# Performance work log

Hardware: AMD Instinct MI355X
Metric: run time of the kernel (lower is better)

## Reference

```python
import jax, jax.numpy as jnp
import numpy as np

NUM_ROIS = 148
BSZ = 16
HID = 64
IN_CH = 128
OUT_CH = 2
N1, E1 = 131072, 2097152
N2, E2 = 2368, 37888
LRELU_SLOPE = 0.01
BN_EPS = 1e-5


def gcn_conv(x, src, dst, ew, W, b, n):
    """PyG GCNConv with edge weights and self-loops (weight 1): D^-1/2 (A+I) D^-1/2 X W + b."""
    h = x @ W  # (n, out)
    deg = jax.ops.segment_sum(ew, dst, num_segments=n) + 1.0  # self-loop weight 1
    dinv = jax.lax.rsqrt(deg)
    norm = dinv[src] * ew * dinv[dst]  # (E,)
    out = jax.ops.segment_sum(h[src] * norm[:, None], dst, num_segments=n)
    out = out + h * (dinv * dinv)[:, None]  # self-loop term: 1/deg
    return out + b


def roi_pool_mean(x, roi, batch, num_rois, bsz):
    """Segment mean keyed by (batch, roi); empty groups stay zero. Returns (bsz, num_rois*d)."""
    seg = batch * num_rois + roi
    nseg = bsz * num_rois
    sums = jax.ops.segment_sum(x, seg, num_segments=nseg)
    cnt = jax.ops.segment_sum(jnp.ones((x.shape[0],), x.dtype), seg, num_segments=nseg)
    pooled = sums / jnp.maximum(cnt, 1.0)[:, None]
    return pooled.reshape(bsz, -1)


def _params(key):
    ks = jax.random.split(key, 8)
    def lin(k, fi, fo):
        return jax.random.normal(k, (fi, fo), jnp.float32) / np.sqrt(fi)
    p = {}
    p["W1a"], p["b1a"] = lin(ks[0], IN_CH, HID), jnp.zeros((HID,), jnp.float32)
    p["W1b"], p["b1b"] = lin(ks[1], HID, HID), jnp.zeros((HID,), jnp.float32)
    p["W2a"], p["b2a"] = lin(ks[2], IN_CH, HID), jnp.zeros((HID,), jnp.float32)
    p["W2b"], p["b2b"] = lin(ks[3], HID, HID), jnp.zeros((HID,), jnp.float32)
    p["Wm1"], p["bm1"] = lin(ks[4], HID * NUM_ROIS, 1000), jnp.zeros((1000,), jnp.float32)
    p["gamma"], p["beta"] = jnp.ones((1000,), jnp.float32), jnp.zeros((1000,), jnp.float32)
    p["bn_mean"], p["bn_var"] = jnp.zeros((1000,), jnp.float32), jnp.ones((1000,), jnp.float32)
    p["Wm2"], p["bm2"] = lin(ks[5], 1000, OUT_CH), jnp.zeros((OUT_CH,), jnp.float32)
    return p


def setup_inputs() -> dict:
    key = jax.random.key(0)
    ks = jax.random.split(key, 12)
    inp = {
        "x1": jax.random.normal(ks[0], (N1, IN_CH), jnp.float32),
        "node_label": jax.random.randint(ks[1], (N1,), 0, NUM_ROIS, jnp.int32),
        "edge_index1": jax.random.randint(ks[2], (2, E1), 0, N1, jnp.int32),
        "edge_weight1": jax.random.uniform(ks[3], (E1,), jnp.float32),
        "batch1": jnp.sort(jax.random.randint(ks[4], (N1,), 0, BSZ, jnp.int32)),
        "x2": jax.random.normal(ks[5], (N2, IN_CH), jnp.float32),
        "roi_label": jax.random.randint(ks[6], (N2,), 0, NUM_ROIS, jnp.int32),
        "edge_index2": jax.random.randint(ks[7], (2, E2), 0, N2, jnp.int32),
        "edge_weight2": jax.random.uniform(ks[8], (E2,), jnp.float32),
        "batch2": jnp.sort(jax.random.randint(ks[9], (N2,), 0, BSZ, jnp.int32)),
    }
    inp.update(_params(ks[10]))
    return inp


def reference(x1, node_label, edge_index1, edge_weight1, batch1,
              x2, roi_label, edge_index2, edge_weight2, batch2,
              W1a, b1a, W1b, b1b, W2a, b2a, W2b, b2b,
              Wm1, bm1, gamma, beta, bn_mean, bn_var, Wm2, bm2):
    # ROI-graph branch (convs_roi[:-1], eval mode: dropout is identity)
    s2, d2 = edge_index2[0], edge_index2[1]
    h2 = jax.nn.relu(gcn_conv(x2, s2, d2, edge_weight2, W2a, b2a, N2))
    h2 = jax.nn.relu(gcn_conv(h2, s2, d2, edge_weight2, W2b, b2b, N2))
    embedding_roi = roi_pool_mean(h2, roi_label, batch2, NUM_ROIS, BSZ)  # (B, 148*HID)
    # fine-grained branch (convs[:-1])
    s1, d1 = edge_index1[0], edge_index1[1]
    h1 = jax.nn.relu(gcn_conv(x1, s1, d1, edge_weight1, W1a, b1a, N1))
    h1 = jax.nn.relu(gcn_conv(h1, s1, d1, edge_weight1, W1b, b1b, N1))
    embedding = roi_pool_mean(h1, node_label, batch1, NUM_ROIS, BSZ)
    # classifier on embedding + embedding_roi
    s = embedding + embedding_roi
    h = s @ Wm1 + bm1
    h = gamma * (h - bn_mean) * jax.lax.rsqrt(bn_var + BN_EPS) + beta  # BatchNorm1d (eval)
    h = jnp.where(h > 0, h, LRELU_SLOPE * h)  # LeakyReLU
    out = h @ Wm2 + bm2  # (B, OUT_CH)
    return out, embedding, embedding_roi, embedding + embedding_roi
```

## Files before the change

kernel.cpp:

```cpp
#include <hip/hip_runtime.h>
#include <hip/hip_fp16.h>

#define N1 131072
#define E1 2097152
#define N2 2368
#define E2 37888
#define NROIS 148
#define BSZ 16
#define HID 64
#define INCH 128
#define NSEG (BSZ*NROIS)
#define SDIM (NROIS*HID)
#define CLS 1000
#define OCH 2

#define KT1 148
#define KCC 64
#define CT1 4
#define SLP 20

#define NB1 512
#define BLK1 512
#define EPB (E1/BLK1)
#define NPB (N1/NB1)
#define P3CAP 5120

#define CW1 ((N1+15)/16)
#define CW2 ((N2+15)/16)
#define PW  ((NSEG+15)/16)

#define T1 (N1/16)
#define T2 (N2/16)
#define GEMMB ((T1+T2)/4)

typedef _Float16 h8 __attribute__((ext_vector_type(8)));
typedef float f4 __attribute__((ext_vector_type(4)));

__device__ __forceinline__ unsigned packh2(float a, float b) {
    return (unsigned)__half_as_ushort(__float2half_rn(a)) |
           ((unsigned)__half_as_ushort(__float2half_rn(b)) << 16);
}

__device__ __forceinline__ void fma_lo(float& a, unsigned hb, float w) {
    asm("v_fma_mix_f32 %0, %1, %2, %0 op_sel:[0,0,0] op_sel_hi:[1,0,0]"
        : "+v"(a) : "v"(hb), "v"(w));
}
__device__ __forceinline__ void fma_hi(float& a, unsigned hb, float w) {
    asm("v_fma_mix_f32 %0, %1, %2, %0 op_sel:[1,0,0] op_sel_hi:[1,0,0]"
        : "+v"(a) : "v"(hb), "v"(w));
}



__global__ void k_hist_dst(int* __restrict__ cnt, const int* __restrict__ dst, int E) {
    int e = blockIdx.x * 256 + threadIdx.x;
    if (e < E) atomicAdd(&cnt[dst[e]], 1);
}

__global__ void k_hist_seg2(int* __restrict__ c1, const int* __restrict__ b1,
                            const int* __restrict__ l1, int n1_,
                            int* __restrict__ c2, const int* __restrict__ b2,
                            const int* __restrict__ l2, int n2_) {
    int i = blockIdx.x * 256 + threadIdx.x;
    if (i < n1_) { atomicAdd(&c1[b1[i] * NROIS + l1[i]], 1); return; }
    int j = i - n1_;
    if (j < n2_) atomicAdd(&c2[b2[j] * NROIS + l2[j]], 1);
}

__global__ void k_scan1(const int* __restrict__ in, int* __restrict__ out,
                        int* __restrict__ part, int n) {
    __shared__ int sh[256];
    int t = threadIdx.x;
    int i0 = blockIdx.x * 1024 + t * 4;
    int v0 = (i0     < n) ? in[i0]     : 0;
    int v1 = (i0 + 1 < n) ? in[i0 + 1] : 0;
    int v2 = (i0 + 2 < n) ? in[i0 + 2] : 0;
    int v3 = (i0 + 3 < n) ? in[i0 + 3] : 0;
    int tot = v0 + v1 + v2 + v3;
    sh[t] = tot; __syncthreads();
    for (int off = 1; off < 256; off <<= 1) {
        int x = 0; if (t >= off) x = sh[t - off];
        __syncthreads();
        if (t >= off) sh[t] += x;
        __syncthreads();
    }
    int excl = sh[t] - tot;
    if (t == 255) part[blockIdx.x] = sh[255];
    if (i0     < n) out[i0]     = excl;
    if (i0 + 1 < n) out[i0 + 1] = excl + v0;
    if (i0 + 2 < n) out[i0 + 2] = excl + v0 + v1;
    if (i0 + 3 < n) out[i0 + 3] = excl + v0 + v1 + v2;
}

__global__ void k_scan2(int* __restrict__ part, int cnt) {
    __shared__ int sh[256];
    int t = threadIdx.x;
    int v = (t < cnt) ? part[t] : 0;
    sh[t] = v; __syncthreads();
    for (int off = 1; off < 256; off <<= 1) {
        int x = 0; if (t >= off) x = sh[t - off];
        __syncthreads();
        if (t >= off) sh[t] += x;
        __syncthreads();
    }
    if (t < cnt) part[t] = sh[t] - v;
}

__global__ void k_scan3(int* __restrict__ out, const int* __restrict__ part, int n, int total) {
    int i = blockIdx.x * 256 + threadIdx.x;
    if (i < n) out[i] += part[i >> 10];
    if (i == 0) out[n] = total;
}

__global__ void k_scan_one(const int* __restrict__ in0, int* __restrict__ out0,
                           int* __restrict__ oo0, int n0,
                           const int* __restrict__ in1, int* __restrict__ out1,
                           int* __restrict__ oo1, int n1_) {
    __shared__ int sh[256];
    __shared__ int carry;
    const int* in; int* out; int* oo; int n;
    if (blockIdx.x == 0) { in = in0; out = out0; oo = oo0; n = n0; }
    else { if (!in1) return; in = in1; out = out1; oo = oo1; n = n1_; }
    int t = threadIdx.x;
    if (t == 0) carry = 0;
    __syncthreads();
    for (int base = 0; base < n; base += 256) {
        int i = base + t;
        int v = (i < n) ? in[i] : 0;
        sh[t] = v; __syncthreads();
        for (int off = 1; off < 256; off <<= 1) {
            int x = 0; if (t >= off) x = sh[t - off];
            __syncthreads();
            if (t >= off) sh[t] += x;
            __syncthreads();
        }
        if (i < n) {
            int e = carry + sh[t] - v;
            out[i] = e;
            if (oo) oo[i] = e;
        }
        __syncthreads();
        if (t == 255) carry += sh[255];
        __syncthreads();
    }
    if (t == 0) out[n] = carry;
}

__global__ void k_fill_edges(int2* __restrict__ edges, int* __restrict__ off,
                             const int* __restrict__ src, const int* __restrict__ dst,
                             const float* __restrict__ ew, int E) {
    int e = blockIdx.x * 256 + threadIdx.x;
    if (e >= E) return;
    int pos = atomicAdd(&off[dst[e]], 1);
    edges[pos] = make_int2(src[e] << 7, __float_as_int(ew[e]));
}

__global__ void k_fill_seg2(int* __restrict__ id1, int* __restrict__ o1,
                            const int* __restrict__ b1, const int* __restrict__ l1, int n1_,
                            int* __restrict__ id2, int* __restrict__ o2,
                            const int* __restrict__ b2, const int* __restrict__ l2, int n2_) {
    int i = blockIdx.x * 256 + threadIdx.x;
    if (i < n1_) {
        int pos = atomicAdd(&o1[b1[i] * NROIS + l1[i]], 1);
        id1[pos] = i << 7;
        return;
    }
    int j = i - n1_;
    if (j < n2_) {
        int pos = atomicAdd(&o2[b2[j] * NROIS + l2[j]], 1);
        id2[pos] = j << 7;
    }
}

__global__ void k_deg_dinv(float* __restrict__ dinv, const int* __restrict__ row,
                           const int2* __restrict__ edges, int n) {
    int d = blockIdx.x * 256 + threadIdx.x;
    if (d >= n) return;
    int a = row[d], b = row[d + 1];
    float s = 1.0f;
    for (int i = a; i < b; i++) s += __int_as_float(edges[i].y);
    dinv[d] = rsqrtf(s);
}


__global__ __launch_bounds__(256) void k_p1(int* __restrict__ bh, const int* __restrict__ dst) {
    __shared__ int cnt[NB1];
    int t = threadIdx.x, blk = blockIdx.x;
    cnt[t] = 0; cnt[t + 256] = 0;
    __syncthreads();
    int base = blk * EPB;
    const int4* d4 = (const int4*)(dst + base);
    for (int i = t; i < EPB / 4; i += 256) {
        int4 d = d4[i];
        atomicAdd(&cnt[d.x >> 8], 1);
        atomicAdd(&cnt[d.y >> 8], 1);
        atomicAdd(&cnt[d.z >> 8], 1);
        atomicAdd(&cnt[d.w >> 8], 1);
    }
    __syncthreads();
    bh[t * BLK1 + blk] = cnt[t];
    bh[(t + 256) * BLK1 + blk] = cnt[t + 256];
}

__global__ __launch_bounds__(256) void k_p2(int2* __restrict__ tmp, const int* __restrict__ obh,
                                            const int* __restrict__ src,
                                            const int* __restrict__ dst,
                                            const float* __restrict__ ew) {
    __shared__ int2 stage[EPB];
    __shared__ unsigned short bkt[EPB];
    __shared__ int cnt[NB1];
    __shared__ int lofs[NB1];
    __shared__ int gdel[NB1];
    __shared__ int cur[NB1];
    __shared__ int sc[256];
    __shared__ int cbr;
    int t = threadIdx.x, blk = blockIdx.x;
    cnt[t] = 0; cnt[t + 256] = 0;
    __syncthreads();
    int base = blk * EPB;
    const int4* d4 = (const int4*)(dst + base);
    for (int i = t; i < EPB / 4; i += 256) {
        int4 d = d4[i];
        atomicAdd(&cnt[d.x >> 8], 1);
        atomicAdd(&cnt[d.y >> 8], 1);
        atomicAdd(&cnt[d.z >> 8], 1);
        atomicAdd(&cnt[d.w >> 8], 1);
    }
    __syncthreads();
    for (int r = 0; r < 2; r++) {
        int v = cnt[r * 256 + t];
        sc[t] = v; __syncthreads();
        for (int off = 1; off < 256; off <<= 1) {
            int x = 0; if (t >= off) x = sc[t - off];
            __syncthreads();
            if (t >= off) sc[t] += x;
            __syncthreads();
        }
        lofs[r * 256 + t] = (r ? cbr : 0) + sc[t] - v;
        if (t == 255 && r == 0) cbr = sc[255];
        __syncthreads();
    }
    for (int b = t; b < NB1; b += 256) {
        int lo = lofs[b];
        cur[b] = lo;
        gdel[b] = obh[b * BLK1 + blk] - lo;
    }
    __syncthreads();
    for (int i = t; i < EPB; i += 256) {
        int e = base + i;
        int d = dst[e];
        int b = d >> 8;
        int p = atomicAdd(&cur[b], 1);
        stage[p] = make_int2(src[e] | ((d & 255) << 17), __float_as_int(ew[e]));
        bkt[p] = (unsigned short)b;
    }
    __syncthreads();
    for (int i = t; i < EPB; i += 256)
        tmp[gdel[bkt[i]] + i] = stage[i];
}

__global__ __launch_bounds__(256) void k_p3(int2* __restrict__ edges, int* __restrict__ row1,
                                            float* __restrict__ dinv1,
                                            const int2* __restrict__ tmp,
                                            const int* __restrict__ obh) {
    __shared__ int2 stage[P3CAP];
    __shared__ int h[NPB];
    __shared__ float ws[NPB];
    __shared__ int sc[256];
    __shared__ int cur[NPB];
    int t = threadIdx.x, b = blockIdx.x;
    h[t] = 0; ws[t] = 0.f;
    __syncthreads();
    int A = obh[b * BLK1];
    int Eend = (b == NB1 - 1) ? E1 : obh[(b + 1) * BLK1];
    int len = Eend - A;
    for (int j = t; j < len; j += 256) {
        int2 ed = tmp[A + j];
        if (j < P3CAP) stage[j] = ed;
        int dl = (ed.x >> 17) & 255;
        atomicAdd(&h[dl], 1);
        atomicAdd(&ws[dl], __int_as_float(ed.y));
    }
    __syncthreads();
    int cnt_ = h[t];
    sc[t] = cnt_; __syncthreads();
    for (int off = 1; off < 256; off <<= 1) {
        int x = 0; if (t >= off) x = sc[t - off];
        __syncthreads();
        if (t >= off) sc[t] += x;
        __syncthreads();
    }
    int excl = sc[t] - cnt_;
    row1[b * NPB + t] = A + excl;
    dinv1[b * NPB + t] = rsqrtf(1.f + ws[t]);
    cur[t] = excl;
    if (b == NB1 - 1 && t == 255) row1[N1] = E1;
    __syncthreads();
    for (int j = t; j < len; j += 256) {
        int2 ed = (j < P3CAP) ? stage[j] : tmp[A + j];
        int dl = (ed.x >> 17) & 255;
        int s = ed.x & 0x1FFFF;
        int p = atomicAdd(&cur[dl], 1);
        edges[A + p] = make_int2(s << 7, ed.y);
    }
}


__device__ __forceinline__ void wfrag(uint4* __restrict__ o, const float* __restrict__ W,
                                      int KCH, int idx) {
    int lane = idx & 63;
    int rest = idx >> 6;
    int ch = rest % KCH;
    int ct = rest / KCH;
    int kr = ch * 32 + ((lane >> 4) * 8);
    int col = ct * 16 + (lane & 15);
    const float* wp = W + (size_t)kr * 64 + col;
    o[idx] = make_uint4(packh2(wp[0],   wp[64]),
                        packh2(wp[128], wp[192]),
                        packh2(wp[256], wp[320]),
                        packh2(wp[384], wp[448]));
}

__global__ void k_wprep(uint4* __restrict__ wf1a, const float* __restrict__ W1a,
                        uint4* __restrict__ wf1b, const float* __restrict__ W1b,
                        uint4* __restrict__ wf2a, const float* __restrict__ W2a,
                        uint4* __restrict__ wf2b, const float* __restrict__ W2b) {
    int idx = blockIdx.x * 256 + threadIdx.x;
    if      (idx < 1024) wfrag(wf1a, W1a, 4, idx);
    else if (idx < 1536) wfrag(wf1b, W1b, 2, idx - 1024);
    else if (idx < 2560) wfrag(wf2a, W2a, 4, idx - 1536);
    else if (idx < 3072) wfrag(wf2b, W2b, 2, idx - 2560);
}

__device__ __forceinline__ h8 loadA(const float* p) {
    float4 a = *(const float4*)p;
    float4 b = *(const float4*)(p + 4);
    union { h8 v; __half h[8]; } u;
    u.h[0] = __float2half_rn(a.x); u.h[1] = __float2half_rn(a.y);
    u.h[2] = __float2half_rn(a.z); u.h[3] = __float2half_rn(a.w);
    u.h[4] = __float2half_rn(b.x); u.h[5] = __float2half_rn(b.y);
    u.h[6] = __float2half_rn(b.z); u.h[7] = __float2half_rn(b.w);
    return u.v;
}
__device__ __forceinline__ h8 loadA(const __half* p) {
    union { h8 v; uint4 u; } u;
    u.u = *(const uint4*)p;
    return u.v;
}

template <int K, typename T>
__global__ __launch_bounds__(256) void k_gemm(__half* __restrict__ out1, const T* __restrict__ x1,
                                              const uint4* __restrict__ wfa,
                                              const float* __restrict__ dva, int t1,
                                              __half* __restrict__ out2, const T* __restrict__ x2,
                                              const uint4* __restrict__ wfb,
                                              const float* __restrict__ dvb, int t2) {
    constexpr int KCH = K / 32;
    int wid = blockIdx.x * 4 + (threadIdx.x >> 6);
    int lane = threadIdx.x & 63;
    __half* out; const T* x; const uint4* wf; const float* dv; int row0;
    if (wid < t1) { out = out1; x = x1; wf = wfa; dv = dva; row0 = wid * 16; }
    else {
        int w2 = wid - t1;
        if (w2 >= t2) return;
        out = out2; x = x2; wf = wfb; dv = dvb; row0 = w2 * 16;
    }
    int lrow = lane & 15, lg = lane >> 4;

    h8 bf[4][KCH];
#pragma unroll
    for (int ct = 0; ct < 4; ct++)
#pragma unroll
        for (int ch = 0; ch < KCH; ch++) {
            union { h8 v; uint4 u; } u;
            u.u = wf[(ct * KCH + ch) * 64 + lane];
            bf[ct][ch] = u.v;
        }

    const T* xr = x + (size_t)(row0 + lrow) * K + lg * 8;
    h8 af[KCH];
#pragma unroll
    for (int ch = 0; ch < KCH; ch++) af[ch] = loadA(xr + ch * 32);

    f4 acc[4];
#pragma unroll
    for (int ct = 0; ct < 4; ct++) acc[ct] = (f4){0.f, 0.f, 0.f, 0.f};
#pragma unroll
    for (int ch = 0; ch < KCH; ch++)
#pragma unroll
        for (int ct = 0; ct < 4; ct++)
            acc[ct] = __builtin_amdgcn_mfma_f32_16x16x32_f16(af[ch], bf[ct][ch], acc[ct], 0, 0, 0);

    float scs[4] = {1.f, 1.f, 1.f, 1.f};
    if (dv) {
#pragma unroll
        for (int r = 0; r < 4; r++) scs[r] = dv[row0 + lg * 4 + r];
    }
#pragma unroll
    for (int ct = 0; ct < 4; ct++)
#pragma unroll
        for (int r = 0; r < 4; r++)
            out[(size_t)(row0 + lg * 4 + r) * 64 + ct * 16 + lrow] =
                __float2half_rn(acc[ct][r] * scs[r]);
}

__device__ __forceinline__ void conv_wave(__half* __restrict__ out, const __half* __restrict__ h,
                                          const int2* __restrict__ edges,
                                          const int* __restrict__ row,
                                          const float* __restrict__ dinv,
                                          const float* __restrict__ bias,
                                          int d0, int n, int lane, int presc) {
    int g  = lane >> 4;
    int fl = lane & 15;
    int eh = fl >> 3;
    int f8 = fl & 7;
    int d  = d0 + g;
    bool vn = d < n;
    int a = 0, b = 0;
    if (vn) { a = row[d]; b = row[d + 1]; }
    const char* hb = (const char*)h + f8 * 16;
    float acc[8] = {0.f,0.f,0.f,0.f,0.f,0.f,0.f,0.f};

    for (int base = a; base < b; base += 16) {
        int sv = 0, wv = 0;
        if (base + fl < b) { int2 e = edges[base + fl]; sv = e.x; wv = e.y; }
        int mm = b - base; if (mm > 16) mm = 16;
        int steps = (mm + 1) >> 1;
        int idx = (g << 4) + eh;
        for (int t = 0; t < steps; t++) {
            int   s = __shfl(sv, idx + (t << 1));
            float w = __int_as_float(__shfl(wv, idx + (t << 1)));
            uint4 hv = *(const uint4*)(hb + (unsigned)s);
            fma_lo(acc[0], hv.x, w); fma_hi(acc[1], hv.x, w);
            fma_lo(acc[2], hv.y, w); fma_hi(acc[3], hv.y, w);
            fma_lo(acc[4], hv.z, w); fma_hi(acc[5], hv.z, w);
            fma_lo(acc[6], hv.w, w); fma_hi(acc[7], hv.w, w);
        }
    }
    float r[8];
#pragma unroll
    for (int f = 0; f < 8; f++) r[f] = acc[f] + __shfl_xor(acc[f], 8);
    if (vn && eh == 0) {
        float di = dinv[d];
        uint4 hd = *(const uint4*)(hb + ((unsigned)d << 7));
        fma_lo(r[0], hd.x, 1.f); fma_hi(r[1], hd.x, 1.f);
        fma_lo(r[2], hd.y, 1.f); fma_hi(r[3], hd.y, 1.f);
        fma_lo(r[4], hd.z, 1.f); fma_hi(r[5], hd.z, 1.f);
        fma_lo(r[6], hd.w, 1.f); fma_hi(r[7], hd.w, 1.f);
        float4 b0 = *(const float4*)(bias + f8 * 8);
        float4 b1 = *(const float4*)(bias + f8 * 8 + 4);
        float osc = presc ? di : 1.f;
        float o0 = fmaxf(di * r[0] + b0.x, 0.f) * osc;
        float o1 = fmaxf(di * r[1] + b0.y, 0.f) * osc;
        float o2 = fmaxf(di * r[2] + b0.z, 0.f) * osc;
        float o3 = fmaxf(di * r[3] + b0.w, 0.f) * osc;
        float o4 = fmaxf(di * r[4] + b1.x, 0.f) * osc;
        float o5 = fmaxf(di * r[5] + b1.y, 0.f) * osc;
        float o6 = fmaxf(di * r[6] + b1.z, 0.f) * osc;
        float o7 = fmaxf(di * r[7] + b1.w, 0.f) * osc;
        uint4 ov;
        ov.x = packh2(o0, o1);
        ov.y = packh2(o2, o3);
        ov.z = packh2(o4, o5);
        ov.w = packh2(o6, o7);
        *(uint4*)(out + (size_t)d * HID + f8 * 8) = ov;
    }
}

__global__ __launch_bounds__(256) void k_conv(__half* __restrict__ o1, const __half* __restrict__ h1,
                                              const int2* __restrict__ e1, const int* __restrict__ r1,
                                              const float* __restrict__ dv1, const float* __restrict__ bi1,
                                              int n1_, int nb1_,
                                              __half* __restrict__ o2, const __half* __restrict__ h2,
                                              const int2* __restrict__ e2, const int* __restrict__ r2,
                                              const float* __restrict__ dv2, const float* __restrict__ bi2,
                                              int n2_, int presc) {
    int blk = blockIdx.x;
    int lane = threadIdx.x & 63;
    int wv = threadIdx.x >> 6;
    if (blk < nb1_) conv_wave(o1, h1, e1, r1, dv1, bi1, blk * 16 + wv * 4, n1_, lane, presc);
    else            conv_wave(o2, h2, e2, r2, dv2, bi2, (blk - nb1_) * 16 + wv * 4, n2_, lane, presc);
}

__device__ __forceinline__ void pool_wave(float* __restrict__ emb, const __half* __restrict__ h,
                                          const int* __restrict__ nodeid,
                                          const int* __restrict__ segrow, int s0, int lane) {
    int g  = lane >> 4;
    int fl = lane & 15;
    int eh = fl >> 3;
    int f8 = fl & 7;
    int s  = s0 + g;
    bool vs = s < NSEG;
    int a = 0, b = 0;
    if (vs) { a = segrow[s]; b = segrow[s + 1]; }
    const char* hb = (const char*)h + f8 * 16;
    float acc[8] = {0.f,0.f,0.f,0.f,0.f,0.f,0.f,0.f};

    for (int base = a; base < b; base += 16) {
        int sv = 0, wv = 0;
        if (base + fl < b) { sv = nodeid[base + fl]; wv = 0x3f800000; }
        int mm = b - base; if (mm > 16) mm = 16;
        int steps = (mm + 1) >> 1;
        int idx = (g << 4) + eh;
        for (int t = 0; t < steps; t++) {
            int   q = __shfl(sv, idx + (t << 1));
            float w = __int_as_float(__shfl(wv, idx + (t << 1)));
            uint4 hv = *(const uint4*)(hb + (unsigned)q);
            fma_lo(acc[0], hv.x, w); fma_hi(acc[1], hv.x, w);
            fma_lo(acc[2], hv.y, w); fma_hi(acc[3], hv.y, w);
            fma_lo(acc[4], hv.z, w); fma_hi(acc[5], hv.z, w);
            fma_lo(acc[6], hv.w, w); fma_hi(acc[7], hv.w, w);
        }
    }
    float r[8];
#pragma unroll
    for (int f = 0; f < 8; f++) r[f] = acc[f] + __shfl_xor(acc[f], 8);
    if (vs && eh == 0) {
        float inv = 1.0f / fmaxf((float)(b - a), 1.0f);
        float4 lo = make_float4(r[0] * inv, r[1] * inv, r[2] * inv, r[3] * inv);
        float4 hi = make_float4(r[4] * inv, r[5] * inv, r[6] * inv, r[7] * inv);
        *(float4*)(emb + (size_t)s * HID + f8 * 8)     = lo;
        *(float4*)(emb + (size_t)s * HID + f8 * 8 + 4) = hi;
    }
}

__global__ __launch_bounds__(256) void k_pool(float* __restrict__ em1, const __half* __restrict__ h1,
                                              const int* __restrict__ id1, const int* __restrict__ sr1,
                                              int nbs,
                                              float* __restrict__ em2, const __half* __restrict__ h2,
                                              const int* __restrict__ id2, const int* __restrict__ sr2) {
    int blk = blockIdx.x;
    int lane = threadIdx.x & 63;
    int wv = threadIdx.x >> 6;
    if (blk < nbs) pool_wave(em1, h1, id1, sr1, blk * 16 + wv * 4, lane);
    else           pool_wave(em2, h2, id2, sr2, (blk - nbs) * 16 + wv * 4, lane);
}


__global__ __launch_bounds__(256) void k_cls(float* __restrict__ part_,
                                             const float* __restrict__ e1,
                                             const float* __restrict__ e2,
                                             float* __restrict__ esum,
                                             const float* __restrict__ Wm1) {
    __shared__ float sl[KCC * SLP];
    int tid = threadIdx.x;
    int kt = blockIdx.x >> 2, ct = blockIdx.x & 3;
    int k0 = kt * KCC;
    bool wr = (ct == 0);
    for (int i = tid; i < KCC * 16; i += 256) {
        int kk = i & (KCC - 1), b = i >> 6;
        int idx = b * SDIM + k0 + kk;
        float v = e1[idx] + e2[idx];
        sl[kk * SLP + b] = v;
        if (wr) esum[idx] = v;
    }
    __syncthreads();
    int c = ct * 256 + tid;
    bool active = c < CLS;
    const float* wp = Wm1 + (size_t)k0 * CLS + c;
    float wv[KCC];
#pragma unroll
    for (int kk = 0; kk < KCC; kk++)
        wv[kk] = active ? wp[(size_t)kk * CLS] : 0.f;
    float acc[16];
#pragma unroll
    for (int b = 0; b < 16; b++) acc[b] = 0.f;
#pragma unroll
    for (int kk = 0; kk < KCC; kk++) {
        float w = wv[kk];
        float4 s0 = *(const float4*)(&sl[kk * SLP + 0]);
        float4 s1 = *(const float4*)(&sl[kk * SLP + 4]);
        float4 s2 = *(const float4*)(&sl[kk * SLP + 8]);
        float4 s3 = *(const float4*)(&sl[kk * SLP + 12]);
        acc[0]  += s0.x * w; acc[1]  += s0.y * w; acc[2]  += s0.z * w; acc[3]  += s0.w * w;
        acc[4]  += s1.x * w; acc[5]  += s1.y * w; acc[6]  += s1.z * w; acc[7]  += s1.w * w;
        acc[8]  += s2.x * w; acc[9]  += s2.y * w; acc[10] += s2.z * w; acc[11] += s2.w * w;
        acc[12] += s3.x * w; acc[13] += s3.y * w; acc[14] += s3.z * w; acc[15] += s3.w * w;
    }
    float* pp = part_ + (size_t)(kt * CT1 + ct) * 16 * 256;
#pragma unroll
    for (int b = 0; b < 16; b++) pp[b * 256 + tid] = acc[b];
}

__global__ void k_credbn(float* __restrict__ hact, const float* __restrict__ part_,
                         const float* __restrict__ bm1, const float* __restrict__ gamma,
                         const float* __restrict__ beta, const float* __restrict__ mean,
                         const float* __restrict__ var) {
    int idx = blockIdx.x * 256 + threadIdx.x;
    if (idx >= BSZ * CLS) return;
    int b = idx / CLS, c = idx % CLS;
    int ct = c >> 8, cl = c & 255;
    float sum = 0.f;
#pragma unroll 8
    for (int kt = 0; kt < KT1; kt++)
        sum += part_[((size_t)(kt * CT1 + ct) * 16 + b) * 256 + cl];
    float t = sum + bm1[c];
    t = gamma[c] * (t - mean[c]) * rsqrtf(var[c] + 1e-5f) + beta[c];
    hact[idx] = t > 0.f ? t : 0.01f * t;
}

__global__ void k_out(float* __restrict__ outp, const float* __restrict__ hact,
                      const float* __restrict__ Wm2, const float* __restrict__ bm2) {
    int b = blockIdx.x;
    int tid = threadIdx.x;
    int o = tid & 1, part = tid >> 1;
    float acc = (part == 0) ? bm2[o] : 0.f;
    for (int k = part; k < CLS; k += 128) acc += hact[b * CLS + k] * Wm2[k * OCH + o];
    unsafeAtomicAdd(&outp[b * OCH + o], acc);
}

extern "C" void kernel_launch(void* const* d_in, const int* in_sizes, int n_in,
                              void* d_out, int out_size, void* d_ws, size_t ws_size,
                              hipStream_t stream) {
    const float* x1  = (const float*)d_in[0];
    const int*   nl  = (const int*)d_in[1];
    const int*   ei1 = (const int*)d_in[2];
    const float* ew1 = (const float*)d_in[3];
    const int*   ba1 = (const int*)d_in[4];
    const float* x2  = (const float*)d_in[5];
    const int*   rl  = (const int*)d_in[6];
    const int*   ei2 = (const int*)d_in[7];
    const float* ew2 = (const float*)d_in[8];
    const int*   ba2 = (const int*)d_in[9];
    const float* W1a = (const float*)d_in[10];
    const float* b1a = (const float*)d_in[11];
    const float* W1b = (const float*)d_in[12];
    const float* b1b = (const float*)d_in[13];
    const float* W2a = (const float*)d_in[14];
    const float* b2a = (const float*)d_in[15];
    const float* W2b = (const float*)d_in[16];
    const float* b2b = (const float*)d_in[17];
    const float* Wm1 = (const float*)d_in[18];
    const float* bm1 = (const float*)d_in[19];
    const float* gam = (const float*)d_in[20];
    const float* bet = (const float*)d_in[21];
    const float* bmn = (const float*)d_in[22];
    const float* bvr = (const float*)d_in[23];
    const float* Wm2 = (const float*)d_in[24];
    const float* bm2 = (const float*)d_in[25];

    float* out  = (float*)d_out;
    float* emb1 = out + 32;
    float* emb2 = emb1 + NSEG * HID;
    float* esum = emb2 + NSEG * HID;

    char* p = (char*)d_ws;
    auto carve = [&](size_t nbytes) { char* q = p; p += (nbytes + 255) & ~(size_t)255; return (void*)q; };
    int*    row1    = (int*)   carve((N1 + 1) * 4);
    int2*   edges1  = (int2*)  carve((size_t)E1 * 8);
    float*  dinv1   = (float*) carve(N1 * 4);
    __half* A1h     = (__half*)carve((size_t)N1 * HID * 2);
    __half* B1h     = (__half*)carve((size_t)N1 * HID * 2);
    int*    nodeid1 = (int*)   carve(N1 * 4);
    int*    segrow1 = (int*)   carve((NSEG + 1) * 4);
    int*    segoff  = (int*)   carve(2 * NSEG * 4);
    int*    bh      = (int*)   carve((NB1 * BLK1 + 1) * 4);
    int*    obh     = (int*)   carve((NB1 * BLK1 + 1) * 4);
    int*    row2    = (int*)   carve((N2 + 1) * 4);
    int*    off2    = (int*)   carve(N2 * 4);
    int2*   edges2  = (int2*)  carve((size_t)E2 * 8);
    float*  dinv2   = (float*) carve(N2 * 4);
    __half* A2h     = (__half*)carve((size_t)N2 * HID * 2);
    __half* B2h     = (__half*)carve((size_t)N2 * HID * 2);
    int*    nodeid2 = (int*)   carve(N2 * 4);
    int*    segrow2 = (int*)   carve((NSEG + 1) * 4);
    int*    part    = (int*)   carve(256 * 4);
    float*  hact    = (float*) carve(BSZ * CLS * 4);
    uint4*  wf1a    = (uint4*) carve(1024 * 16);
    uint4*  wf1b    = (uint4*) carve(512 * 16);
    uint4*  wf2a    = (uint4*) carve(1024 * 16);
    uint4*  wf2b    = (uint4*) carve(512 * 16);
    int*    segoff1 = segoff;
    int*    segoff2 = segoff + NSEG;
    int2*  tmp1 = (int2*)B1h;
    float* clsp = (float*)B1h;

    const int* src1 = ei1;
    const int* dst1 = ei1 + E1;
    const int* src2 = ei2;
    const int* dst2 = ei2 + E2;

    hipMemsetAsync(d_out, 0, (size_t)out_size * sizeof(float), stream);

    k_wprep<<<12, 256, 0, stream>>>(wf1a, W1a, wf1b, W1b, wf2a, W2a, wf2b, W2b);

    hipMemsetAsync(off2, 0, N2 * 4, stream);
    k_hist_dst<<<(E2 + 255) / 256, 256, 0, stream>>>(off2, dst2, E2);
    k_scan_one<<<1, 256, 0, stream>>>(off2, row2, off2, N2, nullptr, nullptr, nullptr, 0);
    k_fill_edges<<<(E2 + 255) / 256, 256, 0, stream>>>(edges2, off2, src2, dst2, ew2, E2);
    k_deg_dinv<<<(N2 + 255) / 256, 256, 0, stream>>>(dinv2, row2, edges2, N2);

    k_p1<<<BLK1, 256, 0, stream>>>(bh, dst1);
    k_scan1<<<(NB1 * BLK1 + 1023) / 1024, 256, 0, stream>>>(bh, obh, part, NB1 * BLK1);
    k_scan2<<<1, 256, 0, stream>>>(part, (NB1 * BLK1 + 1023) / 1024);
    k_scan3<<<(NB1 * BLK1 + 255) / 256, 256, 0, stream>>>(obh, part, NB1 * BLK1, E1);
    k_p2<<<BLK1, 256, 0, stream>>>(tmp1, obh, src1, dst1, ew1);
    k_p3<<<NB1, 256, 0, stream>>>(edges1, row1, dinv1, tmp1, obh);

    k_gemm<INCH, float><<<GEMMB, 256, 0, stream>>>(A1h, x1, wf1a, dinv1, T1,
                                                   A2h, x2, wf2a, dinv2, T2);
    k_conv<<<CW1 + CW2, 256, 0, stream>>>(B1h, A1h, edges1, row1, dinv1, b1a, N1, CW1,
                                          B2h, A2h, edges2, row2, dinv2, b2a, N2, 1);
    k_gemm<HID, __half><<<GEMMB, 256, 0, stream>>>(A1h, B1h, wf1b, nullptr, T1,
                                                   A2h, B2h, wf2b, nullptr, T2);
    k_conv<<<CW1 + CW2, 256, 0, stream>>>(B1h, A1h, edges1, row1, dinv1, b1b, N1, CW1,
                                          B2h, A2h, edges2, row2, dinv2, b2b, N2, 0);

    hipMemsetAsync(segoff, 0, 2 * NSEG * 4, stream);
    k_hist_seg2<<<(N1 + N2 + 255) / 256, 256, 0, stream>>>(segoff1, ba1, nl, N1,
                                                           segoff2, ba2, rl, N2);
    k_scan_one<<<2, 256, 0, stream>>>(segoff1, segrow1, segoff1, NSEG,
                                      segoff2, segrow2, segoff2, NSEG);
    k_fill_seg2<<<(N1 + N2 + 255) / 256, 256, 0, stream>>>(nodeid1, segoff1, ba1, nl, N1,
                                                           nodeid2, segoff2, ba2, rl, N2);
    k_pool<<<PW + PW, 256, 0, stream>>>(emb1, B1h, nodeid1, segrow1, PW,
                                        emb2, B2h, nodeid2, segrow2);

    k_cls<<<KT1 * CT1, 256, 0, stream>>>(clsp, emb1, emb2, esum, Wm1);
    k_credbn<<<(BSZ * CLS + 255) / 256, 256, 0, stream>>>(hact, clsp, bm1, gam, bet, bmn, bvr);
    k_out<<<BSZ, 256, 0, stream>>>(out, hact, Wm2, bm2);
}
```

Measured before the change: 493.6 us.

## Merge small-graph CSR build into big-graph kernels, fuse classifier tail, unroll gathers

The separate small-graph histogram, scan, fill and degree kernels are folded into extra blocks of the large-graph p1/scan2/p2/p3 kernels. The three memsets move into the weight-prep kernel, and the final BN/LeakyReLU kernel now also computes the output projection with wave reductions and atomics, removing k_out and the hact buffer. The conv edge-gather loops are unrolled by two so two neighbor rows load at once. This cuts about eight launches and memsets and adds memory-level parallelism in the gather, at the cost of more atomics in the output and slightly larger kernels.

```diff
diff --git a/kernel.cpp b/kernel.cpp
--- a/kernel.cpp
+++ b/kernel.cpp
@@ -25,6 +25,9 @@
 #define NPB (N1/NB1)
 #define P3CAP 5120
 
+#define G2HB ((E2+255)/256)
+#define G2DB ((N2+255)/256)
+
 #define CW1 ((N1+15)/16)
 #define CW2 ((N2+15)/16)
 #define PW  ((NSEG+15)/16)
@@ -51,11 +54,6 @@
 }
 
 
-
-__global__ void k_hist_dst(int* __restrict__ cnt, const int* __restrict__ dst, int E) {
-    int e = blockIdx.x * 256 + threadIdx.x;
-    if (e < E) atomicAdd(&cnt[dst[e]], 1);
-}
 
 __global__ void k_hist_seg2(int* __restrict__ c1, const int* __restrict__ b1,
                             const int* __restrict__ l1, int n1_,
@@ -92,9 +90,37 @@
     if (i0 + 3 < n) out[i0 + 3] = excl + v0 + v1 + v2;
 }
 
-__global__ void k_scan2(int* __restrict__ part, int cnt) {
+__global__ void k_scan2(int* __restrict__ part, int cnt,
+                        const int* __restrict__ in2, int* __restrict__ out2,
+                        int* __restrict__ oo2, int n2) {
     __shared__ int sh[256];
+    __shared__ int carry;
     int t = threadIdx.x;
+    if (blockIdx.x == 1) {
+        if (t == 0) carry = 0;
+        __syncthreads();
+        for (int base = 0; base < n2; base += 256) {
+            int i = base + t;
+            int v = (i < n2) ? in2[i] : 0;
+            sh[t] = v; __syncthreads();
+            for (int off = 1; off < 256; off <<= 1) {
+                int x = 0; if (t >= off) x = sh[t - off];
+                __syncthreads();
+                if (t >= off) sh[t] += x;
+                __syncthreads();
+            }
+            if (i < n2) {
+                int e = carry + sh[t] - v;
+                out2[i] = e;
+                oo2[i] = e;
+            }
+            __syncthreads();
+            if (t == 255) carry += sh[255];
+            __syncthreads();
+        }
+        if (t == 0) out2[n2] = carry;
+        return;
+    }
     int v = (t < cnt) ? part[t] : 0;
     sh[t] = v; __syncthreads();
     for (int off = 1; off < 256; off <<= 1) {
@@ -146,15 +172,6 @@
     if (t == 0) out[n] = carry;
 }
 
-__global__ void k_fill_edges(int2* __restrict__ edges, int* __restrict__ off,
-                             const int* __restrict__ src, const int* __restrict__ dst,
-                             const float* __restrict__ ew, int E) {
-    int e = blockIdx.x * 256 + threadIdx.x;
-    if (e >= E) return;
-    int pos = atomicAdd(&off[dst[e]], 1);
-    edges[pos] = make_int2(src[e] << 7, __float_as_int(ew[e]));
-}
-
 __global__ void k_fill_seg2(int* __restrict__ id1, int* __restrict__ o1,
                             const int* __restrict__ b1, const int* __restrict__ l1, int n1_,
                             int* __restrict__ id2, int* __restrict__ o2,
@@ -172,20 +189,16 @@
     }
 }
 
-__global__ void k_deg_dinv(float* __restrict__ dinv, const int* __restrict__ row,
-                           const int2* __restrict__ edges, int n) {
-    int d = blockIdx.x * 256 + threadIdx.x;
-    if (d >= n) return;
-    int a = row[d], b = row[d + 1];
-    float s = 1.0f;
-    for (int i = a; i < b; i++) s += __int_as_float(edges[i].y);
-    dinv[d] = rsqrtf(s);
-}
-
-
-__global__ __launch_bounds__(256) void k_p1(int* __restrict__ bh, const int* __restrict__ dst) {
+
+__global__ __launch_bounds__(256) void k_p1(int* __restrict__ bh, const int* __restrict__ dst,
+                                            int* __restrict__ off2, const int* __restrict__ dst2) {
     __shared__ int cnt[NB1];
     int t = threadIdx.x, blk = blockIdx.x;
+    if (blk >= BLK1) {
+        int e = (blk - BLK1) * 256 + t;
+        if (e < E2) atomicAdd(&off2[dst2[e]], 1);
+        return;
+    }
     cnt[t] = 0; cnt[t + 256] = 0;
     __syncthreads();
     int base = blk * EPB;
@@ -205,7 +218,11 @@
 __global__ __launch_bounds__(256) void k_p2(int2* __restrict__ tmp, const int* __restrict__ obh,
                                             const int* __restrict__ src,
                                             const int* __restrict__ dst,
-                                            const float* __restrict__ ew) {
+                                            const float* __restrict__ ew,
+                                            int2* __restrict__ edges2, int* __restrict__ off2,
+                                            const int* __restrict__ src2,
+                                            const int* __restrict__ dst2,
+                                            const float* __restrict__ ew2) {
     __shared__ int2 stage[EPB];
     __shared__ unsigned short bkt[EPB];
     __shared__ int cnt[NB1];
@@ -215,6 +232,14 @@
     __shared__ int sc[256];
     __shared__ int cbr;
     int t = threadIdx.x, blk = blockIdx.x;
+    if (blk >= BLK1) {
+        int e = (blk - BLK1) * 256 + t;
+        if (e < E2) {
+            int pos = atomicAdd(&off2[dst2[e]], 1);
+            edges2[pos] = make_int2(src2[e] << 7, __float_as_int(ew2[e]));
+        }
+        return;
+    }
     cnt[t] = 0; cnt[t + 256] = 0;
     __syncthreads();
     int base = blk * EPB;
@@ -262,13 +287,26 @@
 __global__ __launch_bounds__(256) void k_p3(int2* __restrict__ edges, int* __restrict__ row1,
                                             float* __restrict__ dinv1,
                                             const int2* __restrict__ tmp,
-                                            const int* __restrict__ obh) {
+                                            const int* __restrict__ obh,
+                                            float* __restrict__ dinv2,
+                                            const int* __restrict__ row2,
+                                            const int2* __restrict__ edges2, int n2_) {
     __shared__ int2 stage[P3CAP];
     __shared__ int h[NPB];
     __shared__ float ws[NPB];
     __shared__ int sc[256];
     __shared__ int cur[NPB];
     int t = threadIdx.x, b = blockIdx.x;
+    if (b >= NB1) {
+        int d = (b - NB1) * 256 + t;
+        if (d < n2_) {
+            int a = row2[d], e_ = row2[d + 1];
+            float s = 1.0f;
+            for (int i = a; i < e_; i++) s += __int_as_float(edges2[i].y);
+            dinv2[d] = rsqrtf(s);
+        }
+        return;
+    }
     h[t] = 0; ws[t] = 0.f;
     __syncthreads();
     int A = obh[b * BLK1];
@@ -324,12 +362,17 @@
 __global__ void k_wprep(uint4* __restrict__ wf1a, const float* __restrict__ W1a,
                         uint4* __restrict__ wf1b, const float* __restrict__ W1b,
                         uint4* __restrict__ wf2a, const float* __restrict__ W2a,
-                        uint4* __restrict__ wf2b, const float* __restrict__ W2b) {
+                        uint4* __restrict__ wf2b, const float* __restrict__ W2b,
+                        float* __restrict__ outz, int* __restrict__ off2z,
+                        int* __restrict__ segoffz) {
     int idx = blockIdx.x * 256 + threadIdx.x;
     if      (idx < 1024) wfrag(wf1a, W1a, 4, idx);
     else if (idx < 1536) wfrag(wf1b, W1b, 2, idx - 1024);
     else if (idx < 2560) wfrag(wf2a, W2a, 4, idx - 1536);
     else if (idx < 3072) wfrag(wf2b, W2b, 2, idx - 2560);
+    else if (idx < 3104) outz[idx - 3072] = 0.f;
+    else if (idx < 3104 + N2) off2z[idx - 3104] = 0;
+    else if (idx < 3104 + N2 + 2 * NSEG) segoffz[idx - 3104 - N2] = 0;
 }
 
 __device__ __forceinline__ h8 loadA(const float* p) {
@@ -427,7 +470,24 @@
         int mm = b - base; if (mm > 16) mm = 16;
         int steps = (mm + 1) >> 1;
         int idx = (g << 4) + eh;
-        for (int t = 0; t < steps; t++) {
+        int t = 0;
+        for (; t + 2 <= steps; t += 2) {
+            int   s0 = __shfl(sv, idx + (t << 1));
+            float w0 = __int_as_float(__shfl(wv, idx + (t << 1)));
+            int   s1 = __shfl(sv, idx + (t << 1) + 2);
+            float w1 = __int_as_float(__shfl(wv, idx + (t << 1) + 2));
+            uint4 h0 = *(const uint4*)(hb + (unsigned)s0);
+            uint4 h1 = *(const uint4*)(hb + (unsigned)s1);
+            fma_lo(acc[0], h0.x, w0); fma_hi(acc[1], h0.x, w0);
+            fma_lo(acc[2], h0.y, w0); fma_hi(acc[3], h0.y, w0);
+            fma_lo(acc[4], h0.z, w0); fma_hi(acc[5], h0.z, w0);
+            fma_lo(acc[6], h0.w, w0); fma_hi(acc[7], h0.w, w0);
+            fma_lo(acc[0], h1.x, w1); fma_hi(acc[1], h1.x, w1);
+            fma_lo(acc[2], h1.y, w1); fma_hi(acc[3], h1.y, w1);
+            fma_lo(acc[4], h1.z, w1); fma_hi(acc[5], h1.z, w1);
+            fma_lo(acc[6], h1.w, w1); fma_hi(acc[7], h1.w, w1);
+        }
+        if (t < steps) {
             int   s = __shfl(sv, idx + (t << 1));
             float w = __int_as_float(__shfl(wv, idx + (t << 1)));
             uint4 hv = *(const uint4*)(hb + (unsigned)s);
@@ -502,7 +562,24 @@
         int mm = b - base; if (mm > 16) mm = 16;
         int steps = (mm + 1) >> 1;
         int idx = (g << 4) + eh;
-        for (int t = 0; t < steps; t++) {
+        int t = 0;
+        for (; t + 2 <= steps; t += 2) {
+            int   q0 = __shfl(sv, idx + (t << 1));
+            float w0 = __int_as_float(__shfl(wv, idx + (t << 1)));
+            int   q1 = __shfl(sv, idx + (t << 1) + 2);
+            float w1 = __int_as_float(__shfl(wv, idx + (t << 1) + 2));
+            uint4 h0 = *(const uint4*)(hb + (unsigned)q0);
+            uint4 h1 = *(const uint4*)(hb + (unsigned)q1);
+            fma_lo(acc[0], h0.x, w0); fma_hi(acc[1], h0.x, w0);
+            fma_lo(acc[2], h0.y, w0); fma_hi(acc[3], h0.y, w0);
+            fma_lo(acc[4], h0.z, w0); fma_hi(acc[5], h0.z, w0);
+            fma_lo(acc[6], h0.w, w0); fma_hi(acc[7], h0.w, w0);
+            fma_lo(acc[0], h1.x, w1); fma_hi(acc[1], h1.x, w1);
+            fma_lo(acc[2], h1.y, w1); fma_hi(acc[3], h1.y, w1);
+            fma_lo(acc[4], h1.z, w1); fma_hi(acc[5], h1.z, w1);
+            fma_lo(acc[6], h1.w, w1); fma_hi(acc[7], h1.w, w1);
+        }
+        if (t < steps) {
             int   q = __shfl(sv, idx + (t << 1));
             float w = __int_as_float(__shfl(wv, idx + (t << 1)));
             uint4 hv = *(const uint4*)(hb + (unsigned)q);
@@ -582,31 +659,45 @@
     for (int b = 0; b < 16; b++) pp[b * 256 + tid] = acc[b];
 }
 
-__global__ void k_credbn(float* __restrict__ hact, const float* __restrict__ part_,
+__global__ void k_credbn(float* __restrict__ outp, const float* __restrict__ part_,
                          const float* __restrict__ bm1, const float* __restrict__ gamma,
                          const float* __restrict__ beta, const float* __restrict__ mean,
-                         const float* __restrict__ var) {
+                         const float* __restrict__ var, const float* __restrict__ Wm2,
+                         const float* __restrict__ bm2) {
     int idx = blockIdx.x * 256 + threadIdx.x;
-    if (idx >= BSZ * CLS) return;
-    int b = idx / CLS, c = idx % CLS;
-    int ct = c >> 8, cl = c & 255;
-    float sum = 0.f;
+    float p0 = 0.f, p1 = 0.f;
+    int b = 0;
+    if (idx < BSZ * CLS) {
+        b = idx / CLS;
+        int c = idx % CLS;
+        int ct = c >> 8, cl = c & 255;
+        float sum = 0.f;
 #pragma unroll 8
-    for (int kt = 0; kt < KT1; kt++)
-        sum += part_[((size_t)(kt * CT1 + ct) * 16 + b) * 256 + cl];
-    float t = sum + bm1[c];
-    t = gamma[c] * (t - mean[c]) * rsqrtf(var[c] + 1e-5f) + beta[c];
-    hact[idx] = t > 0.f ? t : 0.01f * t;
-}
-
-__global__ void k_out(float* __restrict__ outp, const float* __restrict__ hact,
-                      const float* __restrict__ Wm2, const float* __restrict__ bm2) {
-    int b = blockIdx.x;
-    int tid = threadIdx.x;
-    int o = tid & 1, part = tid >> 1;
-    float acc = (part == 0) ? bm2[o] : 0.f;
-    for (int k = part; k < CLS; k += 128) acc += hact[b * CLS + k] * Wm2[k * OCH + o];
-    unsafeAtomicAdd(&outp[b * OCH + o], acc);
+        for (int kt = 0; kt < KT1; kt++)
+            sum += part_[((size_t)(kt * CT1 + ct) * 16 + b) * 256 + cl];
+        float t = sum + bm1[c];
+        t = gamma[c] * (t - mean[c]) * rsqrtf(var[c] + 1e-5f) + beta[c];
+        t = t > 0.f ? t : 0.01f * t;
+        p0 = t * Wm2[c * OCH];
+        p1 = t * Wm2[c * OCH + 1];
+        if (c == 0) { p0 += bm2[0]; p1 += bm2[1]; }
+    }
+    int b0 = __shfl(b, 0), b63 = __shfl(b, 63);
+    if (b0 == b63) {
+        float s0 = p0, s1 = p1;
+#pragma unroll
+        for (int off = 32; off >= 1; off >>= 1) {
+            s0 += __shfl_down(s0, off);
+            s1 += __shfl_down(s1, off);
+        }
+        if ((threadIdx.x & 63) == 0 && idx < BSZ * CLS) {
+            unsafeAtomicAdd(&outp[b * OCH],     s0);
+            unsafeAtomicAdd(&outp[b * OCH + 1], s1);
+        }
+    } else if (idx < BSZ * CLS) {
+        unsafeAtomicAdd(&outp[b * OCH],     p0);
+        unsafeAtomicAdd(&outp[b * OCH + 1], p1);
+    }
 }
 
 extern "C" void kernel_launch(void* const* d_in, const int* in_sizes, int n_in,
@@ -665,7 +756,6 @@
     int*    nodeid2 = (int*)   carve(N2 * 4);
     int*    segrow2 = (int*)   carve((NSEG + 1) * 4);
     int*    part    = (int*)   carve(256 * 4);
-    float*  hact    = (float*) carve(BSZ * CLS * 4);
     uint4*  wf1a    = (uint4*) carve(1024 * 16);
     uint4*  wf1b    = (uint4*) carve(512 * 16);
     uint4*  wf2a    = (uint4*) carve(1024 * 16);
@@ -680,22 +770,18 @@
     const int* src2 = ei2;
     const int* dst2 = ei2 + E2;
 
-    hipMemsetAsync(d_out, 0, (size_t)out_size * sizeof(float), stream);
-
-    k_wprep<<<12, 256, 0, stream>>>(wf1a, W1a, wf1b, W1b, wf2a, W2a, wf2b, W2b);
-
-    hipMemsetAsync(off2, 0, N2 * 4, stream);
-    k_hist_dst<<<(E2 + 255) / 256, 256, 0, stream>>>(off2, dst2, E2);
-    k_scan_one<<<1, 256, 0, stream>>>(off2, row2, off2, N2, nullptr, nullptr, nullptr, 0);
-    k_fill_edges<<<(E2 + 255) / 256, 256, 0, stream>>>(edges2, off2, src2, dst2, ew2, E2);
-    k_deg_dinv<<<(N2 + 255) / 256, 256, 0, stream>>>(dinv2, row2, edges2, N2);
-
-    k_p1<<<BLK1, 256, 0, stream>>>(bh, dst1);
+    k_wprep<<<41, 256, 0, stream>>>(wf1a, W1a, wf1b, W1b, wf2a, W2a, wf2b, W2b,
+                                    out, off2, segoff);
+
+    k_p1<<<BLK1 + G2HB, 256, 0, stream>>>(bh, dst1, off2, dst2);
     k_scan1<<<(NB1 * BLK1 + 1023) / 1024, 256, 0, stream>>>(bh, obh, part, NB1 * BLK1);
-    k_scan2<<<1, 256, 0, stream>>>(part, (NB1 * BLK1 + 1023) / 1024);
+    k_scan2<<<2, 256, 0, stream>>>(part, (NB1 * BLK1 + 1023) / 1024,
+                                   off2, row2, off2, N2);
     k_scan3<<<(NB1 * BLK1 + 255) / 256, 256, 0, stream>>>(obh, part, NB1 * BLK1, E1);
-    k_p2<<<BLK1, 256, 0, stream>>>(tmp1, obh, src1, dst1, ew1);
-    k_p3<<<NB1, 256, 0, stream>>>(edges1, row1, dinv1, tmp1, obh);
+    k_p2<<<BLK1 + G2HB, 256, 0, stream>>>(tmp1, obh, src1, dst1, ew1,
+                                          edges2, off2, src2, dst2, ew2);
+    k_p3<<<NB1 + G2DB, 256, 0, stream>>>(edges1, row1, dinv1, tmp1, obh,
+                                         dinv2, row2, edges2, N2);
 
     k_gemm<INCH, float><<<GEMMB, 256, 0, stream>>>(A1h, x1, wf1a, dinv1, T1,
                                                    A2h, x2, wf2a, dinv2, T2);
@@ -706,7 +792,6 @@
     k_conv<<<CW1 + CW2, 256, 0, stream>>>(B1h, A1h, edges1, row1, dinv1, b1b, N1, CW1,
                                           B2h, A2h, edges2, row2, dinv2, b2b, N2, 0);
 
-    hipMemsetAsync(segoff, 0, 2 * NSEG * 4, stream);
     k_hist_seg2<<<(N1 + N2 + 255) / 256, 256, 0, stream>>>(segoff1, ba1, nl, N1,
                                                            segoff2, ba2, rl, N2);
     k_scan_one<<<2, 256, 0, stream>>>(segoff1, segrow1, segoff1, NSEG,
@@ -717,6 +802,6 @@
                                         emb2, B2h, nodeid2, segrow2);
 
     k_cls<<<KT1 * CT1, 256, 0, stream>>>(clsp, emb1, emb2, esum, Wm1);
-    k_credbn<<<(BSZ * CLS + 255) / 256, 256, 0, stream>>>(hact, clsp, bm1, gam, bet, bmn, bvr);
-    k_out<<<BSZ, 256, 0, stream>>>(out, hact, Wm2, bm2);
-}
+    k_credbn<<<(BSZ * CLS + 255) / 256, 256, 0, stream>>>(out, clsp, bm1, gam, bet,
+                                                          bmn, bvr, Wm2, bm2);
+}
```

Result: faster. 459.4 us (-6.9%).
